# Kernel optimization log

Hardware: AMD Instinct MI355X
Metric: run time of the kernel (lower is better)

## Reference

```python
import jax, jax.numpy as jnp
import numpy as np

N = 100000          # nodes
E = 3200000         # edges (avg degree 32)
EPS = 1e-5          # BatchNorm eps
SLOPE = 0.01        # LeakyReLU negative slope


def _glorot(key, shape):
    lim = float(np.sqrt(6.0 / (shape[0] + shape[1])))
    return jax.random.uniform(key, shape, jnp.float32, -lim, lim)


def setup_inputs() -> dict:
    key = jax.random.key(0)
    ks = jax.random.split(key, 8)
    x = jax.random.normal(ks[0], (N, 128), jnp.float32)
    edge_index = jax.random.randint(ks[1], (2, E), 0, N, dtype=jnp.int64)
    W1 = _glorot(ks[2], (128, 256)); b1 = jnp.zeros((256,), jnp.float32)
    W2 = _glorot(ks[3], (256, 512)); b2 = jnp.zeros((512,), jnp.float32)
    g1 = jnp.ones((256,), jnp.float32); be1 = jnp.zeros((256,), jnp.float32)
    g2 = jnp.ones((512,), jnp.float32); be2 = jnp.zeros((512,), jnp.float32)
    Wd1 = _glorot(ks[4], (512, 4096)); bd1 = jnp.zeros((4096,), jnp.float32)
    Wd2 = _glorot(ks[5], (4096, 6)); bd2 = jnp.zeros((6,), jnp.float32)
    return dict(x=x, edge_index=edge_index, W1=W1, b1=b1, W2=W2, b2=b2,
                g1=g1, be1=be1, g2=g2, be2=be2,
                Wd1=Wd1, bd1=bd1, Wd2=Wd2, bd2=bd2)


def gcn_conv(x, src, dst, W, b):
    # PyG GCNConv: x' = D^{-1/2} (A + I) D^{-1/2} (x W) + b
    n = x.shape[0]
    xw = x @ W                                   # [N, out]
    loop = jnp.arange(n, dtype=src.dtype)
    s = jnp.concatenate([src, loop])             # add self-loops
    d = jnp.concatenate([dst, loop])
    deg = jax.ops.segment_sum(jnp.ones_like(d, dtype=x.dtype), d, num_segments=n)
    dinv = jnp.where(deg > 0, jax.lax.rsqrt(deg), 0.0)
    norm = dinv[s] * dinv[d]                     # [E+N]
    out = jax.ops.segment_sum(xw[s] * norm[:, None], d, num_segments=n)
    return out + b


def batchnorm(x, g, b):
    # training-mode BN over node dim, biased variance (as torch)
    m = x.mean(axis=0)
    v = x.var(axis=0)
    return (x - m) * jax.lax.rsqrt(v + EPS) * g + b


def leaky_relu(x):
    return jnp.where(x >= 0, x, SLOPE * x)


def reference(x, edge_index, W1, b1, W2, b2, g1, be1, g2, be2, Wd1, bd1, Wd2, bd2):
    src, dst = edge_index[0], edge_index[1]
    y = leaky_relu(batchnorm(gcn_conv(x, src, dst, W1, b1), g1, be1))
    y = leaky_relu(batchnorm(gcn_conv(y, src, dst, W2, b2), g2, be2))
    y = leaky_relu(y @ Wd1 + bd1)
    y = y @ Wd2 + bd2
    return jax.nn.softmax(y, axis=1)
```

## Files before the change

### kernel.cpp

```cpp
#include <hip/hip_runtime.h>
#include <math.h>

#define LEAKY(t) ((t) >= 0.0f ? (t) : 0.01f * (t))

typedef __attribute__((ext_vector_type(8))) short bf16x8;
typedef __attribute__((ext_vector_type(4))) float f32x4;

static __device__ __forceinline__ float b2f(unsigned short u) {
    return __uint_as_float(((unsigned)u) << 16);
}
static __device__ __forceinline__ unsigned short f2b(float f) {
    unsigned x = __float_as_uint(f);
    unsigned r = (x + 0x7fffu + ((x >> 16) & 1u)) >> 16;
    return (unsigned short)r;
}


__global__ void k_seti(int* __restrict__ p, int v, int n) {
    int i = blockIdx.x * blockDim.x + threadIdx.x;
    int st = gridDim.x * blockDim.x;
    for (; i < n; i += st) p[i] = v;
}

__global__ void k_setf(float* __restrict__ p, float v, int n) {
    int i = blockIdx.x * blockDim.x + threadIdx.x;
    int st = gridDim.x * blockDim.x;
    for (; i < n; i += st) p[i] = v;
}

__global__ void k_stash_f32(const float* __restrict__ a, int i0, int i1, int i2, int i3,
                            float* __restrict__ dst) {
    if (threadIdx.x == 0 && blockIdx.x == 0) {
        dst[0] = a[i0]; dst[1] = a[i1]; dst[2] = a[i2]; dst[3] = a[i3];
    }
}

__global__ void k_stash_b16(const unsigned short* __restrict__ a, int i0, int i1, int i2, int i3,
                            float* __restrict__ dst) {
    if (threadIdx.x == 0 && blockIdx.x == 0) {
        dst[0] = b2f(a[i0]); dst[1] = b2f(a[i1]); dst[2] = b2f(a[i2]); dst[3] = b2f(a[i3]);
    }
}


__global__ void k_detect(const int* __restrict__ ei, int* __restrict__ flag) {
    __shared__ int nz;
    if (threadIdx.x == 0) nz = 0;
    __syncthreads();
    int acc = 0;
    for (int i = threadIdx.x; i < 1024; i += 256) acc |= ei[2 * i + 1];
    if (acc != 0) atomicOr(&nz, 1);
    __syncthreads();
    if (threadIdx.x == 0) *flag = (nz == 0) ? 1 : 0;
}


__global__ void k_count(const int* __restrict__ ei, int E, int Nn,
                        const int* __restrict__ flag, int* __restrict__ cnt) {
    int f = *flag;
    int i = blockIdx.x * blockDim.x + threadIdx.x;
    int stride = gridDim.x * blockDim.x;
    for (; i < E; i += stride) {
        int d = f ? ei[2 * E + 2 * i] : ei[E + i];
        if ((unsigned)d < (unsigned)Nn) atomicAdd(&cnt[d], 1);
    }
}

__global__ void k_dinv(const int* __restrict__ cnt, float* __restrict__ dinv, int n) {
    int i = blockIdx.x * blockDim.x + threadIdx.x;
    if (i < n) dinv[i] = rsqrtf((float)(cnt[i] + 1));
}

__global__ void k_scan(const int* __restrict__ cnt, int* __restrict__ start, int n) {
    __shared__ int sm[256];
    __shared__ int carry;
    int tid = threadIdx.x;
    if (tid == 0) carry = 0;
    __syncthreads();
    for (int base = 0; base < n; base += 1024) {
        int i0 = base + tid * 4;
        int v0 = (i0 + 0 < n) ? cnt[i0 + 0] : 0;
        int v1 = (i0 + 1 < n) ? cnt[i0 + 1] : 0;
        int v2 = (i0 + 2 < n) ? cnt[i0 + 2] : 0;
        int v3 = (i0 + 3 < n) ? cnt[i0 + 3] : 0;
        int s = v0 + v1 + v2 + v3;
        sm[tid] = s;
        __syncthreads();
        int x = s;
        for (int off = 1; off < 256; off <<= 1) {
            int y = (tid >= off) ? sm[tid - off] : 0;
            __syncthreads();
            x += y;
            sm[tid] = x;
            __syncthreads();
        }
        int e = x - s + carry;
        if (i0 + 0 < n) start[i0 + 0] = e; e += v0;
        if (i0 + 1 < n) start[i0 + 1] = e; e += v1;
        if (i0 + 2 < n) start[i0 + 2] = e; e += v2;
        if (i0 + 3 < n) start[i0 + 3] = e; e += v3;
        __syncthreads();
        if (tid == 255) carry += sm[255];
        __syncthreads();
    }
    if (tid == 0) start[n] = carry;
}

__global__ void k_copy_i32(const int* __restrict__ a, int* __restrict__ b, int n) {
    int i = blockIdx.x * blockDim.x + threadIdx.x;
    if (i < n) b[i] = a[i];
}

__global__ void k_fill(const int* __restrict__ ei, int E, int Nn,
                       const int* __restrict__ flag,
                       int* __restrict__ cursor, int* __restrict__ srcS) {
    int f = *flag;
    int i = blockIdx.x * blockDim.x + threadIdx.x;
    int stride = gridDim.x * blockDim.x;
    for (; i < E; i += stride) {
        int s = f ? ei[2 * i] : ei[i];
        int d = f ? ei[2 * E + 2 * i] : ei[E + i];
        if ((unsigned)d < (unsigned)Nn) {
            int p = atomicAdd(&cursor[d], 1);
            srcS[p] = ((unsigned)s < (unsigned)Nn) ? s : 0;
        }
    }
}


__global__ void k_agg1(const float* __restrict__ x, const float* __restrict__ dinv,
                       const int* __restrict__ start, const int* __restrict__ srcS,
                       float* __restrict__ out, int M) {
    int t = threadIdx.x;
    for (int n = blockIdx.x; n < M; n += gridDim.x) {
        float di = dinv[n];
        float a = x[(size_t)n * 128 + t] * di;
        int e1 = start[n + 1];
        for (int j = start[n]; j < e1; ++j) {
            int s = srcS[j];
            a += x[(size_t)s * 128 + t] * dinv[s];
        }
        out[(size_t)n * 128 + t] = a * di;
    }
}

__global__ void k_agg2(const unsigned short* __restrict__ Y1, const float* __restrict__ dinv,
                       const int* __restrict__ start, const int* __restrict__ srcS,
                       unsigned short* __restrict__ T2, int M) {
    int t = threadIdx.x;
    for (int n = blockIdx.x; n < M; n += gridDim.x) {
        float di = dinv[n];
        unsigned v = *(const unsigned*)(Y1 + (size_t)n * 256 + 2 * t);
        float a0 = b2f((unsigned short)(v & 0xffff)) * di;
        float a1 = b2f((unsigned short)(v >> 16)) * di;
        int e1 = start[n + 1];
        for (int j = start[n]; j < e1; ++j) {
            int s = srcS[j];
            float w = dinv[s];
            unsigned u = *(const unsigned*)(Y1 + (size_t)s * 256 + 2 * t);
            a0 += b2f((unsigned short)(u & 0xffff)) * w;
            a1 += b2f((unsigned short)(u >> 16)) * w;
        }
        unsigned o = (unsigned)f2b(a0 * di) | ((unsigned)f2b(a1 * di) << 16);
        *(unsigned*)(T2 + (size_t)n * 256 + 2 * t) = o;
    }
}


__global__ __launch_bounds__(256, 2)
void k_gemm1(const float* __restrict__ A, const unsigned short* __restrict__ W1s,
             unsigned short* __restrict__ C, int M) {
    int tid = threadIdx.x;
    int lane = tid & 63, w = tid >> 6;
    int lr = lane & 15, lg = lane >> 4;
    int row0 = blockIdx.x * 64;
    int arow = row0 + w * 16 + lr;
    const float* Ar = A + (size_t)(arow < M ? arow : (M - 1)) * 128;
    bf16x8 a8[4];
#pragma unroll
    for (int ko = 0; ko < 4; ko++) {
        float4 f0 = *(const float4*)(Ar + ko * 32 + lg * 8);
        float4 f1 = *(const float4*)(Ar + ko * 32 + lg * 8 + 4);
        bf16x8 v;
        v[0] = (short)f2b(f0.x); v[1] = (short)f2b(f0.y);
        v[2] = (short)f2b(f0.z); v[3] = (short)f2b(f0.w);
        v[4] = (short)f2b(f1.x); v[5] = (short)f2b(f1.y);
        v[6] = (short)f2b(f1.z); v[7] = (short)f2b(f1.w);
        a8[ko] = v;
    }
    for (int ct = 0; ct < 16; ct += 2) {
        f32x4 acc0 = {0.f, 0.f, 0.f, 0.f}, acc1 = {0.f, 0.f, 0.f, 0.f};
#pragma unroll
        for (int ko = 0; ko < 4; ko++) {
            const unsigned short* bp = W1s + ((size_t)(ct * 4 + ko) * 64 + lane) * 8;
            bf16x8 b0 = *(const bf16x8*)bp;
            bf16x8 b1 = *(const bf16x8*)(bp + 2048);
            acc0 = __builtin_amdgcn_mfma_f32_16x16x32_bf16(a8[ko], b0, acc0, 0, 0, 0);
            acc1 = __builtin_amdgcn_mfma_f32_16x16x32_bf16(a8[ko], b1, acc1, 0, 0, 0);
        }
        int col = ct * 16 + lr;
#pragma unroll
        for (int i = 0; i < 4; i++) {
            int r = row0 + w * 16 + lg * 4 + i;
            if (r < M) {
                C[(size_t)r * 256 + col] = f2b(acc0[i]);
                C[(size_t)r * 256 + col + 16] = f2b(acc1[i]);
            }
        }
    }
}


__global__ void k_gemm2stats(const unsigned short* __restrict__ T2,
                             const unsigned short* __restrict__ W2s,
                             float* __restrict__ sums, int M) {
    __shared__ float ls[512];
    __shared__ float lq[512];
    int tid = threadIdx.x;
    int lane = tid & 63, w = tid >> 6;
    int lr = lane & 15, lg = lane >> 4;
    int row0 = blockIdx.x * 64;
    for (int i = tid; i < 512; i += 256) { ls[i] = 0.f; lq[i] = 0.f; }
    __syncthreads();

    int arow = row0 + w * 16 + lr;
    bf16x8 a8[8];
    if (arow < M) {
        const unsigned short* T2r = T2 + (size_t)arow * 256;
#pragma unroll
        for (int ko = 0; ko < 8; ko++)
            a8[ko] = *(const bf16x8*)(T2r + ko * 32 + lg * 8);
    } else {
#pragma unroll
        for (int ko = 0; ko < 8; ko++)
            a8[ko] = (bf16x8){0, 0, 0, 0, 0, 0, 0, 0};
    }

    for (int ct = 0; ct < 32; ct += 2) {
        f32x4 acc0 = {0.f, 0.f, 0.f, 0.f}, acc1 = {0.f, 0.f, 0.f, 0.f};
#pragma unroll
        for (int ko = 0; ko < 8; ko++) {
            const unsigned short* bp = W2s + ((size_t)(ct * 8 + ko) * 64 + lane) * 8;
            bf16x8 b0 = *(const bf16x8*)bp;
            bf16x8 b1 = *(const bf16x8*)(bp + 4096);
            acc0 = __builtin_amdgcn_mfma_f32_16x16x32_bf16(a8[ko], b0, acc0, 0, 0, 0);
            acc1 = __builtin_amdgcn_mfma_f32_16x16x32_bf16(a8[ko], b1, acc1, 0, 0, 0);
        }
        float s0 = 0.f, q0 = 0.f, s1 = 0.f, q1 = 0.f;
#pragma unroll
        for (int i = 0; i < 4; i++) {
            float y0 = acc0[i]; s0 += y0; q0 += y0 * y0;
            float y1 = acc1[i]; s1 += y1; q1 += y1 * y1;
        }
        s0 += __shfl_xor(s0, 16); s0 += __shfl_xor(s0, 32);
        q0 += __shfl_xor(q0, 16); q0 += __shfl_xor(q0, 32);
        s1 += __shfl_xor(s1, 16); s1 += __shfl_xor(s1, 32);
        q1 += __shfl_xor(q1, 16); q1 += __shfl_xor(q1, 32);
        if (lg == 0) {
            atomicAdd(&ls[ct * 16 + lr], s0);
            atomicAdd(&lq[ct * 16 + lr], q0);
            atomicAdd(&ls[(ct + 1) * 16 + lr], s1);
            atomicAdd(&lq[(ct + 1) * 16 + lr], q1);
        }
    }
    __syncthreads();
    for (int c = tid; c < 512; c += 256) {
        atomicAdd(&sums[c], ls[c]);
        atomicAdd(&sums[512 + c], lq[c]);
    }
}


__global__ void k_bnparam(float* __restrict__ sums, const float* __restrict__ g,
                          const float* __restrict__ be, int n, int F) {
    int c = blockIdx.x * blockDim.x + threadIdx.x;
    if (c < F) {
        float m = sums[c] / n;
        float v = sums[F + c] / n - m * m;
        float a = g[c] * rsqrtf(v + 1e-5f);
        sums[c] = a;
        sums[F + c] = be[c] - m * a;
    }
}

__global__ void k_colstats_b16(const unsigned short* __restrict__ X, float* __restrict__ sums, int n) {
    int t = threadIdx.x;
    int r0 = blockIdx.x * 256;
    int r1 = min(r0 + 256, n);
    float s = 0.f, q = 0.f;
    for (int r = r0; r < r1; r++) {
        float v = b2f(X[(size_t)r * 256 + t]);
        s += v; q += v * v;
    }
    atomicAdd(&sums[t], s);
    atomicAdd(&sums[256 + t], q);
}

__global__ void k_bnleaky_b16(unsigned short* __restrict__ X, const float* __restrict__ p,
                              long long total) {
    long long i = (long long)blockIdx.x * blockDim.x + threadIdx.x;
    long long stride = (long long)gridDim.x * blockDim.x;
    for (; i < total; i += stride) {
        int c = (int)(i & 255);
        float y = b2f(X[i]) * p[c] + p[256 + c];
        X[i] = f2b(LEAKY(y));
    }
}


__global__ void k_swz(const float* __restrict__ src, unsigned short* __restrict__ dst,
                      int N, int KO) {
    __shared__ float t[32][65];
    int tid = threadIdx.x;
    int ko = blockIdx.x;
    int n0 = blockIdx.y * 64;
    int r = tid >> 3, c8 = (tid & 7) * 8;
    const float* s = src + (size_t)(ko * 32 + r) * N + n0 + c8;
    float4 v0 = *(const float4*)s;
    float4 v1 = *(const float4*)(s + 4);
    t[r][c8 + 0] = v0.x; t[r][c8 + 1] = v0.y; t[r][c8 + 2] = v0.z; t[r][c8 + 3] = v0.w;
    t[r][c8 + 4] = v1.x; t[r][c8 + 5] = v1.y; t[r][c8 + 6] = v1.z; t[r][c8 + 7] = v1.w;
    __syncthreads();
    int cc = tid >> 6, lane = tid & 63;
    int lr = lane & 15, lg = lane >> 4;
    int ct = (n0 >> 4) + cc;
    bf16x8 ov;
#pragma unroll
    for (int j = 0; j < 8; j++) ov[j] = (short)f2b(t[lg * 8 + j][cc * 16 + lr]);
    *(bf16x8*)(dst + ((size_t)(ct * KO + ko) * 64 + lane) * 8) = ov;
}


__global__ __launch_bounds__(256, 2)
void k_dense(const unsigned short* __restrict__ T2,
             const unsigned short* __restrict__ W2s,
             const float* __restrict__ bnp,
             const float* __restrict__ bd1,
             const unsigned short* __restrict__ Wd1s,
             const float* __restrict__ Wd2,
             float* __restrict__ logits, int M) {
    __shared__ unsigned short Y2[64][520];
    __shared__ float sl[2][64][6];
    int tid = threadIdx.x;
    int lane = tid & 63, w = tid >> 6;
    int lr = lane & 15, lg = lane >> 4;
    int row0 = blockIdx.x * 64;

    int arow = row0 + w * 16 + lr;
    const unsigned short* T2r = T2 + (size_t)(arow < M ? arow : (M - 1)) * 256;
    bf16x8 a8[8];
#pragma unroll
    for (int ko = 0; ko < 8; ko++)
        a8[ko] = *(const bf16x8*)(T2r + ko * 32 + lg * 8);
    for (int ct = 0; ct < 32; ct += 2) {
        f32x4 acc0 = {0.f, 0.f, 0.f, 0.f}, acc1 = {0.f, 0.f, 0.f, 0.f};
#pragma unroll
        for (int ko = 0; ko < 8; ko++) {
            const unsigned short* bp = W2s + ((size_t)(ct * 8 + ko) * 64 + lane) * 8;
            bf16x8 b0 = *(const bf16x8*)bp;
            bf16x8 b1 = *(const bf16x8*)(bp + 4096);
            acc0 = __builtin_amdgcn_mfma_f32_16x16x32_bf16(a8[ko], b0, acc0, 0, 0, 0);
            acc1 = __builtin_amdgcn_mfma_f32_16x16x32_bf16(a8[ko], b1, acc1, 0, 0, 0);
        }
        int col = ct * 16 + lr;
        float sc0 = bnp[col], sh0 = bnp[512 + col];
        float sc1 = bnp[col + 16], sh1 = bnp[512 + col + 16];
#pragma unroll
        for (int i = 0; i < 4; i++) {
            float y0 = fmaf(acc0[i], sc0, sh0); y0 = LEAKY(y0);
            Y2[w * 16 + lg * 4 + i][col] = f2b(y0);
            float y1 = fmaf(acc1[i], sc1, sh1); y1 = LEAKY(y1);
            Y2[w * 16 + lg * 4 + i][col + 16] = f2b(y1);
        }
    }
    __syncthreads();

    int rg = w & 1, ch = w >> 1;
    bf16x8 pA[16], pB[16];
#pragma unroll
    for (int ko = 0; ko < 16; ko++) {
        pA[ko] = *(const bf16x8*)(&Y2[rg * 32 + lr][ko * 32 + lg * 8]);
        pB[ko] = *(const bf16x8*)(&Y2[rg * 32 + 16 + lr][ko * 32 + lg * 8]);
    }
    float l0[4][6] = {{0.f}}, l1[4][6] = {{0.f}};
    int ct0 = ch * 128;
    for (int ct = ct0; ct < ct0 + 128; ++ct) {
        f32x4 acc0 = {0.f, 0.f, 0.f, 0.f}, acc1 = {0.f, 0.f, 0.f, 0.f};
#pragma unroll
        for (int ko = 0; ko < 16; ko++) {
            bf16x8 b = *(const bf16x8*)(Wd1s + ((size_t)(ct * 16 + ko) * 64 + lane) * 8);
            acc0 = __builtin_amdgcn_mfma_f32_16x16x32_bf16(pA[ko], b, acc0, 0, 0, 0);
            acc1 = __builtin_amdgcn_mfma_f32_16x16x32_bf16(pB[ko], b, acc1, 0, 0, 0);
        }
        int col = ct * 16 + lr;
        float bv = bd1[col];
        const float* w2r = Wd2 + (size_t)col * 6;
        float u0 = w2r[0], u1 = w2r[1], u2 = w2r[2];
        float u3 = w2r[3], u4 = w2r[4], u5 = w2r[5];
#pragma unroll
        for (int i = 0; i < 4; i++) {
            float t0 = acc0[i] + bv; t0 = LEAKY(t0);
            l0[i][0] = fmaf(t0, u0, l0[i][0]);
            l0[i][1] = fmaf(t0, u1, l0[i][1]);
            l0[i][2] = fmaf(t0, u2, l0[i][2]);
            l0[i][3] = fmaf(t0, u3, l0[i][3]);
            l0[i][4] = fmaf(t0, u4, l0[i][4]);
            l0[i][5] = fmaf(t0, u5, l0[i][5]);
            float t1 = acc1[i] + bv; t1 = LEAKY(t1);
            l1[i][0] = fmaf(t1, u0, l1[i][0]);
            l1[i][1] = fmaf(t1, u1, l1[i][1]);
            l1[i][2] = fmaf(t1, u2, l1[i][2]);
            l1[i][3] = fmaf(t1, u3, l1[i][3]);
            l1[i][4] = fmaf(t1, u4, l1[i][4]);
            l1[i][5] = fmaf(t1, u5, l1[i][5]);
        }
    }
#pragma unroll
    for (int i = 0; i < 4; i++) {
#pragma unroll
        for (int o = 0; o < 6; o++) {
            float v0 = l0[i][o];
            v0 += __shfl_xor(v0, 1); v0 += __shfl_xor(v0, 2);
            v0 += __shfl_xor(v0, 4); v0 += __shfl_xor(v0, 8);
            float v1 = l1[i][o];
            v1 += __shfl_xor(v1, 1); v1 += __shfl_xor(v1, 2);
            v1 += __shfl_xor(v1, 4); v1 += __shfl_xor(v1, 8);
            if (lr == 0) {
                sl[ch][rg * 32 + lg * 4 + i][o] = v0;
                sl[ch][rg * 32 + 16 + lg * 4 + i][o] = v1;
            }
        }
    }
    __syncthreads();
    for (int i = tid; i < 384; i += 256) {
        int r = i / 6, o = i - r * 6;
        if (row0 + r < M)
            logits[(size_t)(row0 + r) * 6 + o] = sl[0][r][o] + sl[1][r][o];
    }
}


__global__ void k_softmax(const float* __restrict__ logits, const float* __restrict__ bd2,
                          float* __restrict__ out, int M) {
    int n = blockIdx.x * blockDim.x + threadIdx.x;
    if (n >= M) return;
    float l[6];
    float mx = -1e30f;
#pragma unroll
    for (int o = 0; o < 6; o++) {
        l[o] = logits[(size_t)n * 6 + o] + bd2[o];
        mx = fmaxf(mx, l[o]);
    }
    float s = 0.f;
#pragma unroll
    for (int o = 0; o < 6; o++) { l[o] = expf(l[o] - mx); s += l[o]; }
    float inv = 1.f / s;
#pragma unroll
    for (int o = 0; o < 6; o++) out[(size_t)n * 6 + o] = l[o] * inv;
}


__global__ void k_diag_ws(float* __restrict__ out, unsigned long long ws) {
    if (threadIdx.x == 0 && blockIdx.x == 0) {
        float f = (float)((double)ws / 1099511627776.0);
        if (f > 0.999f) f = 0.999f;
        out[0] = ldexpf(1.0f + f, 34);
    }
}

__global__ void k_diag(const int* __restrict__ eflag, const int* __restrict__ startM,
                       int E, const float* __restrict__ stash,
                       const float* __restrict__ logits, float* __restrict__ out) {
    if (threadIdx.x != 0 || blockIdx.x != 0) return;
    int b1 = *eflag;
    int b2 = (*startM == E) ? 1 : 0;
    int b3 = (fabsf(stash[0] - stash[1]) > 1e-12f || fabsf(stash[2] - stash[3]) > 1e-12f) ? 1 : 0;
    int b4 = (fabsf(stash[4]) > 1e-12f || fabsf(stash[5]) > 1e-12f ||
              fabsf(stash[6]) > 1e-12f || fabsf(stash[7]) > 1e-12f) ? 1 : 0;
    float d0 = fabsf(logits[0] - logits[6]);
    float d1 = fabsf(logits[0] - logits[1]);
    int b5 = (d0 > 1e-12f && d1 > 1e-12f) ? 1 : 0;
    if (b2 && b3 && b4 && b5) return;
    float meanabs = 0.f;
    for (int i = 0; i < 16; i++) meanabs += fabsf(logits[i]);
    meanabs *= (1.f / 16.f);
    int m = (int)(32.f + 8.f * log2f(meanabs + 1e-30f));
    m = m < 0 ? 0 : (m > 127 ? 127 : m);
    int Ee = 96 + 16 * b1 + 8 * b2 + 4 * b3 + 2 * b4 + b5;
    out[0] = ldexpf(1.0f + (float)m / 128.0f, Ee - 30);
}


extern "C" void kernel_launch(void* const* d_in, const int* in_sizes, int n_in,
                              void* d_out, int out_size, void* d_ws, size_t ws_size,
                              hipStream_t stream) {
    const float* x   = (const float*)d_in[0];
    const int*   ei  = (const int*)d_in[1];
    const float* W1  = (const float*)d_in[2];
    const float* W2  = (const float*)d_in[4];
    const float* g1  = (const float*)d_in[6];
    const float* be1 = (const float*)d_in[7];
    const float* g2  = (const float*)d_in[8];
    const float* be2 = (const float*)d_in[9];
    const float* Wd1 = (const float*)d_in[10];
    const float* bd1 = (const float*)d_in[11];
    const float* Wd2 = (const float*)d_in[12];
    const float* bd2 = (const float*)d_in[13];
    float* out = (float*)d_out;

    const int M = in_sizes[0] / 128;
    const int E = in_sizes[1] / 2;

    size_t szA = (size_t)M * 512;
    size_t szB = (size_t)M * 512;
    size_t csr = (size_t)M * 8 + ((size_t)M + 1) * 8 + (size_t)E * 4 + 8192 + 128 + 66000;
    size_t need = szA + szB + csr;

    if (ws_size < need) {
        k_setf<<<2048, 256, 0, stream>>>(out, 0.f, out_size);
        k_diag_ws<<<1, 64, 0, stream>>>(out, (unsigned long long)ws_size);
        return;
    }

    char* base = (char*)d_ws;
    float* T1 = (float*)base;
    unsigned short* T2 = (unsigned short*)base;
    unsigned short* Y1 = (unsigned short*)(base + szA);
    float* logits = (float*)(base + szA);
    unsigned short* W2s  = (unsigned short*)(base + szA + (size_t)8 * 1024 * 1024);
    unsigned short* Wd1s = (unsigned short*)(base + szA + (size_t)12 * 1024 * 1024);
    char* cb = base + szA + szB;
    float* dinv   = (float*)cb;
    int*   cnt    = (int*)(dinv + M);
    int*   startA = cnt + M;
    int*   cursor = startA + (M + 1);
    int*   srcS   = cursor + (M + 1);
    float* sums   = (float*)(srcS + E);
    int*   eflag  = (int*)(sums + 2048);
    float* stash  = (float*)(eflag + 8);
    unsigned short* W1s = (unsigned short*)(((uintptr_t)(stash + 16) + 63) & ~(uintptr_t)63);

    int mt  = (M + 63) / 64;
    int nb  = (M + 255) / 256;

    k_detect<<<1, 256, 0, stream>>>(ei, eflag);
    k_seti<<<2048, 256, 0, stream>>>(cnt, 0, M);
    k_count<<<4096, 256, 0, stream>>>(ei, E, M, eflag, cnt);
    k_dinv<<<nb, 256, 0, stream>>>(cnt, dinv, M);
    k_scan<<<1, 256, 0, stream>>>(cnt, startA, M);
    k_copy_i32<<<nb, 256, 0, stream>>>(startA, cursor, M);
    k_fill<<<4096, 256, 0, stream>>>(ei, E, M, eflag, cursor, srcS);
    k_swz<<<dim3(4, 4), 256, 0, stream>>>(W1, W1s, 256, 4);

    k_agg1<<<4096, 128, 0, stream>>>(x, dinv, startA, srcS, T1, M);
    k_stash_f32<<<1, 64, 0, stream>>>(T1, 3, 128 * 7 + 3, 0, 128 * 7, stash);
    k_gemm1<<<mt, 256, 0, stream>>>(T1, W1s, Y1, M);
    k_setf<<<8, 256, 0, stream>>>(sums, 0.f, 2048);
    k_colstats_b16<<<nb, 256, 0, stream>>>(Y1, sums, M);
    k_bnparam<<<1, 256, 0, stream>>>(sums, g1, be1, M, 256);
    k_bnleaky_b16<<<4096, 256, 0, stream>>>(Y1, sums, (long long)M * 256);
    k_stash_b16<<<1, 64, 0, stream>>>(Y1, 5, 77, 256 + 5, 256 * 9 + 5, stash + 4);

    k_agg2<<<4096, 128, 0, stream>>>(Y1, dinv, startA, srcS, T2, M);
    k_swz<<<dim3(8, 8), 256, 0, stream>>>(W2, W2s, 512, 8);
    k_swz<<<dim3(16, 64), 256, 0, stream>>>(Wd1, Wd1s, 4096, 16);
    k_setf<<<8, 256, 0, stream>>>(sums, 0.f, 2048);
    k_gemm2stats<<<mt, 256, 0, stream>>>(T2, W2s, sums, M);
    k_bnparam<<<2, 256, 0, stream>>>(sums, g2, be2, M, 512);

    k_dense<<<mt, 256, 0, stream>>>(T2, W2s, sums, bd1, Wd1s, Wd2, logits, M);
    k_softmax<<<nb, 256, 0, stream>>>(logits, bd2, out, M);

    k_diag<<<1, 64, 0, stream>>>(eflag, startA + M, E, stash, logits, out);
}
```

Before: 2.742 ms.

## Convert input features to bf16 before first aggregation and unify gather kernels

Adds a pass that converts x to bf16 up front, so the layer-1 neighbour gather reads half the bytes per edge and writes a bf16 aggregate that the first GEMM loads directly instead of converting on the fly. Both aggregation passes now share one kernel that gathers two neighbours per iteration to keep more loads in flight. The dense kernel's A-fragment arrays are replaced with named registers and a macro-unrolled MFMA loop to avoid indexing or spilling. This trades extra rounding of x and the aggregate to bf16 for lower gather traffic, plus one extra conversion kernel.

```diff
diff --git a/kernel.cpp b/kernel.cpp
--- a/kernel.cpp
+++ b/kernel.cpp
@@ -28,17 +28,23 @@
     for (; i < n; i += st) p[i] = v;
 }
 
-__global__ void k_stash_f32(const float* __restrict__ a, int i0, int i1, int i2, int i3,
-                            float* __restrict__ dst) {
-    if (threadIdx.x == 0 && blockIdx.x == 0) {
-        dst[0] = a[i0]; dst[1] = a[i1]; dst[2] = a[i2]; dst[3] = a[i3];
-    }
-}
-
 __global__ void k_stash_b16(const unsigned short* __restrict__ a, int i0, int i1, int i2, int i3,
                             float* __restrict__ dst) {
     if (threadIdx.x == 0 && blockIdx.x == 0) {
         dst[0] = b2f(a[i0]); dst[1] = b2f(a[i1]); dst[2] = b2f(a[i2]); dst[3] = b2f(a[i3]);
+    }
+}
+
+
+__global__ void k_cvt(const float* __restrict__ src, unsigned short* __restrict__ dst,
+                      long long n4) {
+    long long i = (long long)blockIdx.x * blockDim.x + threadIdx.x;
+    long long st = (long long)gridDim.x * blockDim.x;
+    for (; i < n4; i += st) {
+        float4 v = *(const float4*)(src + 4 * i);
+        ushort4 o;
+        o.x = f2b(v.x); o.y = f2b(v.y); o.z = f2b(v.z); o.w = f2b(v.w);
+        *(ushort4*)(dst + 4 * i) = o;
     }
 }
 
@@ -128,66 +134,52 @@
 }
 
 
-__global__ void k_agg1(const float* __restrict__ x, const float* __restrict__ dinv,
+__global__ void k_aggb(const unsigned short* __restrict__ X, const float* __restrict__ dinv,
                        const int* __restrict__ start, const int* __restrict__ srcS,
-                       float* __restrict__ out, int M) {
+                       unsigned short* __restrict__ out, int F, int M) {
     int t = threadIdx.x;
     for (int n = blockIdx.x; n < M; n += gridDim.x) {
         float di = dinv[n];
-        float a = x[(size_t)n * 128 + t] * di;
-        int e1 = start[n + 1];
-        for (int j = start[n]; j < e1; ++j) {
-            int s = srcS[j];
-            a += x[(size_t)s * 128 + t] * dinv[s];
-        }
-        out[(size_t)n * 128 + t] = a * di;
-    }
-}
-
-__global__ void k_agg2(const unsigned short* __restrict__ Y1, const float* __restrict__ dinv,
-                       const int* __restrict__ start, const int* __restrict__ srcS,
-                       unsigned short* __restrict__ T2, int M) {
-    int t = threadIdx.x;
-    for (int n = blockIdx.x; n < M; n += gridDim.x) {
-        float di = dinv[n];
-        unsigned v = *(const unsigned*)(Y1 + (size_t)n * 256 + 2 * t);
+        unsigned v = *(const unsigned*)(X + (size_t)n * F + 2 * t);
         float a0 = b2f((unsigned short)(v & 0xffff)) * di;
         float a1 = b2f((unsigned short)(v >> 16)) * di;
-        int e1 = start[n + 1];
-        for (int j = start[n]; j < e1; ++j) {
-            int s = srcS[j];
-            float w = dinv[s];
-            unsigned u = *(const unsigned*)(Y1 + (size_t)s * 256 + 2 * t);
-            a0 += b2f((unsigned short)(u & 0xffff)) * w;
-            a1 += b2f((unsigned short)(u >> 16)) * w;
+        int j = start[n], e1 = start[n + 1];
+        for (; j + 1 < e1; j += 2) {
+            int s0 = srcS[j], s1 = srcS[j + 1];
+            float w0 = dinv[s0], w1 = dinv[s1];
+            unsigned u0 = *(const unsigned*)(X + (size_t)s0 * F + 2 * t);
+            unsigned u1 = *(const unsigned*)(X + (size_t)s1 * F + 2 * t);
+            a0 += b2f((unsigned short)(u0 & 0xffff)) * w0;
+            a1 += b2f((unsigned short)(u0 >> 16)) * w0;
+            a0 += b2f((unsigned short)(u1 & 0xffff)) * w1;
+            a1 += b2f((unsigned short)(u1 >> 16)) * w1;
+        }
+        if (j < e1) {
+            int s0 = srcS[j];
+            float w0 = dinv[s0];
+            unsigned u0 = *(const unsigned*)(X + (size_t)s0 * F + 2 * t);
+            a0 += b2f((unsigned short)(u0 & 0xffff)) * w0;
+            a1 += b2f((unsigned short)(u0 >> 16)) * w0;
         }
         unsigned o = (unsigned)f2b(a0 * di) | ((unsigned)f2b(a1 * di) << 16);
-        *(unsigned*)(T2 + (size_t)n * 256 + 2 * t) = o;
+        *(unsigned*)(out + (size_t)n * F + 2 * t) = o;
     }
 }
 
 
 __global__ __launch_bounds__(256, 2)
-void k_gemm1(const float* __restrict__ A, const unsigned short* __restrict__ W1s,
+void k_gemm1(const unsigned short* __restrict__ A, const unsigned short* __restrict__ W1s,
              unsigned short* __restrict__ C, int M) {
     int tid = threadIdx.x;
     int lane = tid & 63, w = tid >> 6;
     int lr = lane & 15, lg = lane >> 4;
     int row0 = blockIdx.x * 64;
     int arow = row0 + w * 16 + lr;
-    const float* Ar = A + (size_t)(arow < M ? arow : (M - 1)) * 128;
+    const unsigned short* Ar = A + (size_t)(arow < M ? arow : (M - 1)) * 128;
     bf16x8 a8[4];
 #pragma unroll
-    for (int ko = 0; ko < 4; ko++) {
-        float4 f0 = *(const float4*)(Ar + ko * 32 + lg * 8);
-        float4 f1 = *(const float4*)(Ar + ko * 32 + lg * 8 + 4);
-        bf16x8 v;
-        v[0] = (short)f2b(f0.x); v[1] = (short)f2b(f0.y);
-        v[2] = (short)f2b(f0.z); v[3] = (short)f2b(f0.w);
-        v[4] = (short)f2b(f1.x); v[5] = (short)f2b(f1.y);
-        v[6] = (short)f2b(f1.z); v[7] = (short)f2b(f1.w);
-        a8[ko] = v;
-    }
+    for (int ko = 0; ko < 4; ko++)
+        a8[ko] = *(const bf16x8*)(Ar + ko * 32 + lg * 8);
     for (int ct = 0; ct < 16; ct += 2) {
         f32x4 acc0 = {0.f, 0.f, 0.f, 0.f}, acc1 = {0.f, 0.f, 0.f, 0.f};
 #pragma unroll
@@ -376,22 +368,39 @@
     __syncthreads();
 
     int rg = w & 1, ch = w >> 1;
-    bf16x8 pA[16], pB[16];
-#pragma unroll
-    for (int ko = 0; ko < 16; ko++) {
-        pA[ko] = *(const bf16x8*)(&Y2[rg * 32 + lr][ko * 32 + lg * 8]);
-        pB[ko] = *(const bf16x8*)(&Y2[rg * 32 + 16 + lr][ko * 32 + lg * 8]);
-    }
+    const unsigned short* rowA = &Y2[rg * 32 + lr][0];
+    const unsigned short* rowB = &Y2[rg * 32 + 16 + lr][0];
+    int co = lg * 8;
+    bf16x8 pA0 = *(const bf16x8*)(rowA + 0 * 32 + co),  pB0 = *(const bf16x8*)(rowB + 0 * 32 + co);
+    bf16x8 pA1 = *(const bf16x8*)(rowA + 1 * 32 + co),  pB1 = *(const bf16x8*)(rowB + 1 * 32 + co);
+    bf16x8 pA2 = *(const bf16x8*)(rowA + 2 * 32 + co),  pB2 = *(const bf16x8*)(rowB + 2 * 32 + co);
+    bf16x8 pA3 = *(const bf16x8*)(rowA + 3 * 32 + co),  pB3 = *(const bf16x8*)(rowB + 3 * 32 + co);
+    bf16x8 pA4 = *(const bf16x8*)(rowA + 4 * 32 + co),  pB4 = *(const bf16x8*)(rowB + 4 * 32 + co);
+    bf16x8 pA5 = *(const bf16x8*)(rowA + 5 * 32 + co),  pB5 = *(const bf16x8*)(rowB + 5 * 32 + co);
+    bf16x8 pA6 = *(const bf16x8*)(rowA + 6 * 32 + co),  pB6 = *(const bf16x8*)(rowB + 6 * 32 + co);
+    bf16x8 pA7 = *(const bf16x8*)(rowA + 7 * 32 + co),  pB7 = *(const bf16x8*)(rowB + 7 * 32 + co);
+    bf16x8 pA8 = *(const bf16x8*)(rowA + 8 * 32 + co),  pB8 = *(const bf16x8*)(rowB + 8 * 32 + co);
+    bf16x8 pA9 = *(const bf16x8*)(rowA + 9 * 32 + co),  pB9 = *(const bf16x8*)(rowB + 9 * 32 + co);
+    bf16x8 pA10 = *(const bf16x8*)(rowA + 10 * 32 + co), pB10 = *(const bf16x8*)(rowB + 10 * 32 + co);
+    bf16x8 pA11 = *(const bf16x8*)(rowA + 11 * 32 + co), pB11 = *(const bf16x8*)(rowB + 11 * 32 + co);
+    bf16x8 pA12 = *(const bf16x8*)(rowA + 12 * 32 + co), pB12 = *(const bf16x8*)(rowB + 12 * 32 + co);
+    bf16x8 pA13 = *(const bf16x8*)(rowA + 13 * 32 + co), pB13 = *(const bf16x8*)(rowB + 13 * 32 + co);
+    bf16x8 pA14 = *(const bf16x8*)(rowA + 14 * 32 + co), pB14 = *(const bf16x8*)(rowB + 14 * 32 + co);
+    bf16x8 pA15 = *(const bf16x8*)(rowA + 15 * 32 + co), pB15 = *(const bf16x8*)(rowB + 15 * 32 + co);
+
     float l0[4][6] = {{0.f}}, l1[4][6] = {{0.f}};
     int ct0 = ch * 128;
     for (int ct = ct0; ct < ct0 + 128; ++ct) {
         f32x4 acc0 = {0.f, 0.f, 0.f, 0.f}, acc1 = {0.f, 0.f, 0.f, 0.f};
-#pragma unroll
-        for (int ko = 0; ko < 16; ko++) {
-            bf16x8 b = *(const bf16x8*)(Wd1s + ((size_t)(ct * 16 + ko) * 64 + lane) * 8);
-            acc0 = __builtin_amdgcn_mfma_f32_16x16x32_bf16(pA[ko], b, acc0, 0, 0, 0);
-            acc1 = __builtin_amdgcn_mfma_f32_16x16x32_bf16(pB[ko], b, acc1, 0, 0, 0);
-        }
+        const unsigned short* bp = Wd1s + ((size_t)(ct * 16) * 64 + lane) * 8;
+#define DSTEP(K, PA, PB) { bf16x8 b = *(const bf16x8*)(bp + (K) * 512); \
+        acc0 = __builtin_amdgcn_mfma_f32_16x16x32_bf16(PA, b, acc0, 0, 0, 0); \
+        acc1 = __builtin_amdgcn_mfma_f32_16x16x32_bf16(PB, b, acc1, 0, 0, 0); }
+        DSTEP(0, pA0, pB0)   DSTEP(1, pA1, pB1)   DSTEP(2, pA2, pB2)   DSTEP(3, pA3, pB3)
+        DSTEP(4, pA4, pB4)   DSTEP(5, pA5, pB5)   DSTEP(6, pA6, pB6)   DSTEP(7, pA7, pB7)
+        DSTEP(8, pA8, pB8)   DSTEP(9, pA9, pB9)   DSTEP(10, pA10, pB10) DSTEP(11, pA11, pB11)
+        DSTEP(12, pA12, pB12) DSTEP(13, pA13, pB13) DSTEP(14, pA14, pB14) DSTEP(15, pA15, pB15)
+#undef DSTEP
         int col = ct * 16 + lr;
         float bv = bd1[col];
         const float* w2r = Wd2 + (size_t)col * 6;
@@ -523,8 +532,9 @@
     }
 
     char* base = (char*)d_ws;
-    float* T1 = (float*)base;
-    unsigned short* T2 = (unsigned short*)base;
+    unsigned short* xb  = (unsigned short*)base;
+    unsigned short* T1b = (unsigned short*)base + (size_t)M * 128;
+    unsigned short* T2  = (unsigned short*)base;
     unsigned short* Y1 = (unsigned short*)(base + szA);
     float* logits = (float*)(base + szA);
     unsigned short* W2s  = (unsigned short*)(base + szA + (size_t)8 * 1024 * 1024);
@@ -550,18 +560,19 @@
     k_scan<<<1, 256, 0, stream>>>(cnt, startA, M);
     k_copy_i32<<<nb, 256, 0, stream>>>(startA, cursor, M);
     k_fill<<<4096, 256, 0, stream>>>(ei, E, M, eflag, cursor, srcS);
+    k_cvt<<<2048, 256, 0, stream>>>(x, xb, (long long)M * 32);
     k_swz<<<dim3(4, 4), 256, 0, stream>>>(W1, W1s, 256, 4);
 
-    k_agg1<<<4096, 128, 0, stream>>>(x, dinv, startA, srcS, T1, M);
-    k_stash_f32<<<1, 64, 0, stream>>>(T1, 3, 128 * 7 + 3, 0, 128 * 7, stash);
-    k_gemm1<<<mt, 256, 0, stream>>>(T1, W1s, Y1, M);
+    k_aggb<<<8192, 64, 0, stream>>>(xb, dinv, startA, srcS, T1b, 128, M);
+    k_stash_b16<<<1, 64, 0, stream>>>(T1b, 3, 128 * 7 + 3, 1, 128 * 7, stash);
+    k_gemm1<<<mt, 256, 0, stream>>>(T1b, W1s, Y1, M);
     k_setf<<<8, 256, 0, stream>>>(sums, 0.f, 2048);
     k_colstats_b16<<<nb, 256, 0, stream>>>(Y1, sums, M);
     k_bnparam<<<1, 256, 0, stream>>>(sums, g1, be1, M, 256);
     k_bnleaky_b16<<<4096, 256, 0, stream>>>(Y1, sums, (long long)M * 256);
     k_stash_b16<<<1, 64, 0, stream>>>(Y1, 5, 77, 256 + 5, 256 * 9 + 5, stash + 4);
 
-    k_agg2<<<4096, 128, 0, stream>>>(Y1, dinv, startA, srcS, T2, M);
+    k_aggb<<<4096, 128, 0, stream>>>(Y1, dinv, startA, srcS, T2, 256, M);
     k_swz<<<dim3(8, 8), 256, 0, stream>>>(W2, W2s, 512, 8);
     k_swz<<<dim3(16, 64), 256, 0, stream>>>(Wd1, Wd1s, 4096, 16);
     k_setf<<<8, 256, 0, stream>>>(sums, 0.f, 2048);
```

Result: faster. 2.624 ms (-4.3%).
